# Kernel tuning notes

Hardware: AMD Instinct MI355X
Metric: run time of the kernel (lower is better)

Reference implementation:

```python
import jax, jax.numpy as jnp
import numpy as np

N = 50000      # nodes
E = 800000     # edges (avg degree 16)
F_IN = 128     # in_channels
H = 4          # heads
C = 32         # hidden_channels (per-head out)
L = 3          # num_layers
HC = H * C     # 128 == F_IN so residuals are active


def _layer_norm(x, g, b):
    mu = jnp.mean(x, axis=-1, keepdims=True)
    var = jnp.mean(jnp.square(x - mu), axis=-1, keepdims=True)
    return (x - mu) * jax.lax.rsqrt(var + 1e-5) * g + b


def _gatv2(x, W_l, b_l, W_r, b_r, att, src, dst, concat):
    # GATv2Conv (PyG semantics, eval mode: no dropout)
    xl = (x @ W_l + b_l).reshape(-1, H, C)   # source-side transform  [N,H,C]
    xr = (x @ W_r + b_r).reshape(-1, H, C)   # target-side transform  [N,H,C]
    e = jax.nn.leaky_relu(xl[src] + xr[dst], 0.2)          # [E,H,C]
    alpha = jnp.einsum('ehc,hc->eh', e, att)               # [E,H]
    # segment softmax over incoming edges of each dst node
    m = jax.ops.segment_max(alpha, dst, num_segments=N)    # [N,H]
    a = jnp.exp(alpha - m[dst])
    den = jax.ops.segment_sum(a, dst, num_segments=N) + 1e-16
    a = a / den[dst]
    out = jax.ops.segment_sum(xl[src] * a[:, :, None], dst, num_segments=N)  # [N,H,C]
    if concat:
        return out.reshape(N, HC)
    return out.mean(axis=1)


def setup_inputs() -> dict:
    key = jax.random.key(0)
    ks = jax.random.split(key, 6)
    s = 0.05
    return {
        "x": jax.random.normal(ks[0], (N, F_IN), jnp.float32),
        "edge_index": jax.random.randint(ks[1], (2, E), 0, N, dtype=jnp.int32),
        # all 3 layers have in=128, out=H*C=128 for the linears
        "Wl": jax.random.normal(ks[2], (L, F_IN, HC), jnp.float32) * s,
        "bl": jnp.zeros((L, HC), jnp.float32),
        "Wr": jax.random.normal(ks[3], (L, F_IN, HC), jnp.float32) * s,
        "br": jnp.zeros((L, HC), jnp.float32),
        "att": jax.random.normal(ks[4], (L, H, C), jnp.float32) * s,
        "out_bias01": jnp.zeros((2, HC), jnp.float32),   # concat layers 0,1
        "out_bias2": jnp.zeros((C,), jnp.float32),       # mean layer 2
        "ln_g01": jnp.ones((2, HC), jnp.float32),
        "ln_b01": jnp.zeros((2, HC), jnp.float32),
        "ln_g2": jnp.ones((C,), jnp.float32),
        "ln_b2": jnp.zeros((C,), jnp.float32),
    }


def reference(x, edge_index, Wl, bl, Wr, br, att,
              out_bias01, out_bias2, ln_g01, ln_b01, ln_g2, ln_b2):
    src, dst = edge_index[0], edge_index[1]
    for i in range(L):
        x_in = x
        concat = i < L - 1
        h = _gatv2(x, Wl[i], bl[i], Wr[i], br[i], att[i], src, dst, concat)
        if concat:
            h = h + out_bias01[i]
            h = _layer_norm(h, ln_g01[i], ln_b01[i])
        else:
            h = h + out_bias2
            h = _layer_norm(h, ln_g2, ln_b2)
        h = jax.nn.relu(h)  # dropout omitted (eval mode)
        if i > 0 and h.shape == x_in.shape:
            h = h + x_in
        x = h
    return x
```

## Files before the change

kernel.cpp:

```cpp
#include <hip/hip_runtime.h>
#include <math.h>


#define DPP_QP_XOR1 0xB1
#define DPP_QP_XOR2 0x4E
#define DPP_ROW_MIRROR 0x140
#define DPP_ROW_HALF_MIRROR 0x141

#define EPB 8192
#define MAXB 512
#define ECAP 4096
#define SCAP 4096

template <int CTRL>
__device__ __forceinline__ float dpp_add(float v) {
    int x = __builtin_amdgcn_update_dpp(0, __float_as_int(v), CTRL, 0xf, 0xf, true);
    return v + __int_as_float(x);
}

__device__ __forceinline__ unsigned bf16s(float f) {
    unsigned u = __float_as_uint(f);
    return (u + 0x7fffu + ((u >> 16) & 1u)) >> 16;
}

typedef __bf16 bf16x8 __attribute__((ext_vector_type(8)));
typedef float f32x4 __attribute__((ext_vector_type(4)));
typedef float f32x2 __attribute__((ext_vector_type(2)));


__global__ __launch_bounds__(256) void bin_kernel(
    const int* __restrict__ src, const int* __restrict__ dst,
    int* __restrict__ bucket_count, unsigned* __restrict__ ebuf,
    int E, int NB)
{
    __shared__ int hist[MAXB], lbase[MAXB], gbase[MAXB], cur[MAXB];
    __shared__ int sscan[256];
    __shared__ unsigned stage[EPB];
    const int t = threadIdx.x;
    const int base = blockIdx.x * EPB;
    const int cnt = min(EPB, E - base);

    for (int b = t; b < MAXB; b += 256) hist[b] = 0;
    __syncthreads();
    for (int idx = t; idx < cnt; idx += 256)
        atomicAdd(&hist[dst[base + idx] >> 7], 1);
    __syncthreads();
    {
        const int a = hist[2 * t], b = hist[2 * t + 1];
        sscan[t] = a + b;
        __syncthreads();
        for (int off = 1; off < 256; off <<= 1) {
            int u = (t >= off) ? sscan[t - off] : 0;
            __syncthreads();
            sscan[t] += u;
            __syncthreads();
        }
        const int ex = sscan[t] - (a + b);
        lbase[2 * t] = ex;
        lbase[2 * t + 1] = ex + a;
    }
    __syncthreads();
    for (int b = t; b < NB; b += 256) {
        const int c = hist[b];
        gbase[b] = (c > 0) ? atomicAdd(&bucket_count[b], c) : 0;
        cur[b] = lbase[b];
    }
    __syncthreads();
    for (int idx = t; idx < cnt; idx += 256) {
        const int d = dst[base + idx];
        const int bk = d >> 7;
        const int lp = atomicAdd(&cur[bk], 1);
        stage[lp] = (unsigned)src[base + idx] | ((unsigned)(d & 127) << 16)
                  | ((unsigned)bk << 23);
    }
    __syncthreads();
    for (int idx = t; idx < cnt; idx += 256) {
        const unsigned v = stage[idx];
        const int bk = v >> 23;
        ebuf[(size_t)bk * ECAP + gbase[bk] + (idx - lbase[bk])] = v;
    }
}


__global__ __launch_bounds__(256) void place_kernel(
    const unsigned* __restrict__ ebuf, const int* __restrict__ bucket_count,
    int* __restrict__ row_start, int* __restrict__ deg,
    unsigned short* __restrict__ src_sorted, int Nn, int NB)
{
    __shared__ int hist[128], lexcl[128], cur[128], s[128];
    __shared__ int ptotS;
    __shared__ unsigned short stage[SCAP];
    const int b = blockIdx.x;
    const int t = threadIdx.x;
    const int node0 = b * 128;
    const int cnt = min(bucket_count[b], ECAP);
    const unsigned* eb = ebuf + (size_t)b * ECAP;

    if (t < 128) hist[t] = 0;
    __syncthreads();
    for (int i = t; i < cnt; i += 256)
        atomicAdd(&hist[(eb[i] >> 16) & 127], 1);
    __syncthreads();
    int pv = 0;
    if (t < 128) { pv = (hist[t] + 3) & ~3; s[t] = pv; }
    __syncthreads();
    for (int off = 1; off < 128; off <<= 1) {
        int u = (t >= off && t < 128) ? s[t - off] : 0;
        __syncthreads();
        if (t < 128) s[t] += u;
        __syncthreads();
    }
    if (t < 128) {
        lexcl[t] = s[t] - pv;
        cur[t] = s[t] - pv;
        const int n = node0 + t;
        if (n < Nn) {
            row_start[n] = b * SCAP + lexcl[t];
            deg[n] = hist[t];
        }
    }
    if (t == 127) ptotS = s[127];
    __syncthreads();
    const int ptot = ptotS;
    for (int i = t; i < ptot; i += 256) stage[i] = 0;
    __syncthreads();
    for (int i = t; i < cnt; i += 256) {
        const unsigned v = eb[i];
        const int lp = atomicAdd(&cur[(v >> 16) & 127], 1);
        stage[lp] = (unsigned short)(v & 0xffffu);
    }
    __syncthreads();
    for (int i = t; i < ptot; i += 256)
        src_sorted[(size_t)b * SCAP + i] = stage[i];
}


__global__ __launch_bounds__(256) void prep_kernel(
    const float* __restrict__ Wl, const float* __restrict__ Wr,
    unsigned short* __restrict__ Bt, int* __restrict__ bucket_cnt, int btTotal)
{
    const int idx = blockIdx.x * blockDim.x + threadIdx.x;
    if (idx < MAXB) bucket_cnt[idx] = 0;
    if (idx < btTotal) {
        const int k = idx & 127;
        const int n = (idx >> 7) & 255;
        const int l = idx >> 15;
        const float v = (n < 128) ? Wl[l * 16384 + k * 128 + n]
                                  : Wr[l * 16384 + k * 128 + (n - 128)];
        Bt[idx] = (unsigned short)bf16s(v);
    }
}


template <bool F32A>
__global__ __launch_bounds__(256) void gemm_mfma(
    const void* __restrict__ Xv, const unsigned short* __restrict__ Bt,
    const float* __restrict__ bl, const float* __restrict__ br,
    unsigned short* __restrict__ XLb, unsigned short* __restrict__ XRb, int Nn)
{
    const int t = threadIdx.x;
    const int lane = t & 63;
    const int w = t >> 6;
    const int n0 = w * 64;
    const int l15 = lane & 15;
    const int kg = lane >> 4;
    const int rowBase = blockIdx.x * 32;

    f32x4 acc[2][4] = {};

    int ra[2];
    ra[0] = min(rowBase + l15, Nn - 1);
    ra[1] = min(rowBase + 16 + l15, Nn - 1);

#pragma unroll
    for (int ks = 0; ks < 4; ++ks) {
        const int k0 = ks * 32 + kg * 8;
        bf16x8 a[2];
#pragma unroll
        for (int mt = 0; mt < 2; ++mt) {
            if constexpr (F32A) {
                const float* X = (const float*)Xv;
                const float4 f0 = *reinterpret_cast<const float4*>(X + (size_t)ra[mt] * 128 + k0);
                const float4 f1 = *reinterpret_cast<const float4*>(X + (size_t)ra[mt] * 128 + k0 + 4);
                bf16x8 av;
                av[0] = (__bf16)f0.x; av[1] = (__bf16)f0.y;
                av[2] = (__bf16)f0.z; av[3] = (__bf16)f0.w;
                av[4] = (__bf16)f1.x; av[5] = (__bf16)f1.y;
                av[6] = (__bf16)f1.z; av[7] = (__bf16)f1.w;
                a[mt] = av;
            } else {
                const unsigned short* Xb = (const unsigned short*)Xv;
                a[mt] = *reinterpret_cast<const bf16x8*>(Xb + (size_t)ra[mt] * 128 + k0);
            }
        }
#pragma unroll
        for (int nt = 0; nt < 4; ++nt) {
            const int col = n0 + nt * 16 + l15;
            const bf16x8 b = *reinterpret_cast<const bf16x8*>(Bt + (size_t)col * 128 + k0);
            acc[0][nt] = __builtin_amdgcn_mfma_f32_16x16x32_bf16(a[0], b, acc[0][nt], 0, 0, 0);
            acc[1][nt] = __builtin_amdgcn_mfma_f32_16x16x32_bf16(a[1], b, acc[1][nt], 0, 0, 0);
        }
    }

    const bool isXL = (w < 2);
#pragma unroll
    for (int mt = 0; mt < 2; ++mt) {
#pragma unroll
        for (int nt = 0; nt < 4; ++nt) {
            const int col = n0 + nt * 16 + l15;
            const float bv = isXL ? bl[col] : br[col - 128];
#pragma unroll
            for (int r = 0; r < 4; ++r) {
                const int row = rowBase + mt * 16 + kg * 4 + r;
                if (row >= Nn) continue;
                const float v = acc[mt][nt][r] + bv;
                if (isXL) XLb[(size_t)row * 128 + col] = (unsigned short)bf16s(v);
                else      XRb[(size_t)row * 128 + (col - 128)] = (unsigned short)bf16s(v);
            }
        }
    }
}


__device__ __forceinline__ void unpack8(const uint4 q, f32x2* v) {
    v[0] = f32x2{__uint_as_float(q.x << 16), __uint_as_float(q.x & 0xffff0000u)};
    v[1] = f32x2{__uint_as_float(q.y << 16), __uint_as_float(q.y & 0xffff0000u)};
    v[2] = f32x2{__uint_as_float(q.z << 16), __uint_as_float(q.z & 0xffff0000u)};
    v[3] = f32x2{__uint_as_float(q.w << 16), __uint_as_float(q.w & 0xffff0000u)};
}

__device__ __forceinline__ void edge_accum(const uint4 q, const f32x2* xr, const f32x2* av,
                                           const bool dead, float& wsum, f32x2* acc) {
    f32x2 xl[4];
    unpack8(q, xl);
    f32x2 pd = {0.f, 0.f};
#pragma unroll
    for (int j = 0; j < 4; ++j) {
        f32x2 tt = xl[j] + xr[j];
        tt = __builtin_elementwise_max(tt, tt * 0.2f);
        pd += tt * av[j];
    }
    float part = pd.x + pd.y;
    part = dpp_add<DPP_QP_XOR1>(part);
    part = dpp_add<DPP_QP_XOR2>(part);
    if (dead) part = -INFINITY;
    const float e = __expf(part);
    wsum += e;
    const f32x2 e2 = {e, e};
#pragma unroll
    for (int j = 0; j < 4; ++j) acc[j] += e2 * xl[j];
}

template <int MODE>
__global__ __launch_bounds__(256, 8) void aggregate_kernel(
    const unsigned* __restrict__ XLb, const unsigned* __restrict__ XRb,
    const int* __restrict__ row_start, const int* __restrict__ deg,
    const unsigned short* __restrict__ src_sorted,
    const float* __restrict__ att, const float* __restrict__ obias,
    const float* __restrict__ lng, const float* __restrict__ lnb,
    const unsigned* __restrict__ residb, float* __restrict__ out,
    unsigned* __restrict__ outb, int Nn)
{
    const int lane = threadIdx.x & 63;
    const int wid = threadIdx.x >> 6;
    const int node = blockIdx.x * 4 + wid;
    if (node >= Nn) return;
    const int g = lane >> 4;
    const int i = lane & 15;
    const int c0 = i * 8;

    f32x2 xr[4], av[4];
    {
        const uint4 qr = reinterpret_cast<const uint4*>(XRb)[(size_t)node * 16 + i];
        unpack8(qr, xr);
        const float4 c = *reinterpret_cast<const float4*>(att + c0);
        const float4 d = *reinterpret_cast<const float4*>(att + c0 + 4);
        av[0] = f32x2{c.x, c.y}; av[1] = f32x2{c.z, c.w};
        av[2] = f32x2{d.x, d.y}; av[3] = f32x2{d.z, d.w};
    }

    f32x2 acc[4] = {};
    float wsum = 0.f;

    const int p0 = row_start[node];
    const int dg = deg[node];
    const int p1 = p0 + dg;
    const uint4* XL4 = reinterpret_cast<const uint4*>(XLb);

    if (dg > 0) {
        uint4 qA = XL4[(size_t)src_sorted[p0 + g] * 16 + i];
        uint4 qB = XL4[(size_t)src_sorted[p0 + 4 + g] * 16 + i];
        for (int p = p0; p < p1; p += 8) {
            const int sAn = src_sorted[p + 8 + g];
            const int sBn = src_sorted[p + 12 + g];
            const uint4 qAn = XL4[(size_t)sAn * 16 + i];
            const uint4 qBn = XL4[(size_t)sBn * 16 + i];
            edge_accum(qA, xr, av, p + g >= p1, wsum, acc);
            if (p + 4 < p1)
                edge_accum(qB, xr, av, p + 4 + g >= p1, wsum, acc);
            qA = qAn;
            qB = qBn;
        }
    }

    wsum += __shfl_xor(wsum, 16); wsum += __shfl_xor(wsum, 32);
    float o[8];
#pragma unroll
    for (int j = 0; j < 4; ++j) { o[2 * j] = acc[j].x; o[2 * j + 1] = acc[j].y; }
#pragma unroll
    for (int j = 0; j < 8; ++j) {
        o[j] += __shfl_xor(o[j], 16);
        o[j] += __shfl_xor(o[j], 32);
    }

    const float inv = 1.f / (wsum + 1e-16f);
#pragma unroll
    for (int j = 0; j < 8; ++j) o[j] *= inv;

    if (MODE < 2) {
        float v[8], d[8];
        float s = 0.f;
#pragma unroll
        for (int j = 0; j < 8; ++j) { v[j] = o[j] + obias[c0 + j]; s += v[j]; }
        s = dpp_add<DPP_QP_XOR1>(s); s = dpp_add<DPP_QP_XOR2>(s);
        s = dpp_add<DPP_ROW_MIRROR>(s); s = dpp_add<DPP_ROW_HALF_MIRROR>(s);
        const float mu = s * (1.f / 128.f);
        float q = 0.f;
#pragma unroll
        for (int j = 0; j < 8; ++j) { d[j] = v[j] - mu; q = fmaf(d[j], d[j], q); }
        q = dpp_add<DPP_QP_XOR1>(q); q = dpp_add<DPP_QP_XOR2>(q);
        q = dpp_add<DPP_ROW_MIRROR>(q); q = dpp_add<DPP_ROW_HALF_MIRROR>(q);
        const float rstd = rsqrtf(q * (1.f / 128.f) + 1e-5f);
        float h[8];
#pragma unroll
        for (int j = 0; j < 8; ++j)
            h[j] = fmaxf(d[j] * rstd * lng[c0 + j] + lnb[c0 + j], 0.f);
        if (MODE == 1) {
            const uint4 qr2 = reinterpret_cast<const uint4*>(residb)[(size_t)node * 16 + i];
            f32x2 rr[4];
            unpack8(qr2, rr);
            h[0] += rr[0].x; h[1] += rr[0].y; h[2] += rr[1].x; h[3] += rr[1].y;
            h[4] += rr[2].x; h[5] += rr[2].y; h[6] += rr[3].x; h[7] += rr[3].y;
        }
        if (g == 0) {
            uint4 pb;
            pb.x = bf16s(h[0]) | (bf16s(h[1]) << 16);
            pb.y = bf16s(h[2]) | (bf16s(h[3]) << 16);
            pb.z = bf16s(h[4]) | (bf16s(h[5]) << 16);
            pb.w = bf16s(h[6]) | (bf16s(h[7]) << 16);
            reinterpret_cast<uint4*>(outb)[(size_t)node * 16 + i] = pb;
        }
    } else {
#pragma unroll
        for (int j = 0; j < 8; ++j) {
            o[j] += __shfl_xor(o[j], 4);
            o[j] += __shfl_xor(o[j], 8);
            o[j] *= 0.25f;
        }
        const int cb = (i & 3) * 8;
        float v[8], d[8];
        float s = 0.f;
#pragma unroll
        for (int j = 0; j < 8; ++j) { v[j] = o[j] + obias[cb + j]; s += v[j]; }
        s = dpp_add<DPP_QP_XOR1>(s); s = dpp_add<DPP_QP_XOR2>(s);
        const float mu = s * (1.f / 32.f);
        float q = 0.f;
#pragma unroll
        for (int j = 0; j < 8; ++j) { d[j] = v[j] - mu; q = fmaf(d[j], d[j], q); }
        q = dpp_add<DPP_QP_XOR1>(q); q = dpp_add<DPP_QP_XOR2>(q);
        const float rstd = rsqrtf(q * (1.f / 32.f) + 1e-5f);
        float h[8];
#pragma unroll
        for (int j = 0; j < 8; ++j)
            h[j] = fmaxf(d[j] * rstd * lng[cb + j] + lnb[cb + j], 0.f);
        if (lane < 4) {
            *reinterpret_cast<float4*>(out + (size_t)node * 32 + cb) =
                make_float4(h[0], h[1], h[2], h[3]);
            *reinterpret_cast<float4*>(out + (size_t)node * 32 + cb + 4) =
                make_float4(h[4], h[5], h[6], h[7]);
        }
    }
}

extern "C" void kernel_launch(void* const* d_in, const int* in_sizes, int n_in,
                              void* d_out, int out_size, void* d_ws, size_t ws_size,
                              hipStream_t stream)
{
    const float* x    = (const float*)d_in[0];
    const int*   ei   = (const int*)d_in[1];
    const float* Wl   = (const float*)d_in[2];
    const float* bl   = (const float*)d_in[3];
    const float* Wr   = (const float*)d_in[4];
    const float* br   = (const float*)d_in[5];
    const float* att  = (const float*)d_in[6];
    const float* ob01 = (const float*)d_in[7];
    const float* ob2  = (const float*)d_in[8];
    const float* lg01 = (const float*)d_in[9];
    const float* lb01 = (const float*)d_in[10];
    const float* lg2  = (const float*)d_in[11];
    const float* lb2  = (const float*)d_in[12];
    float* outp = (float*)d_out;

    const int Nn = in_sizes[0] / 128;
    const int E  = in_sizes[1] / 2;
    const int* srcI = ei;
    const int* dstI = ei + E;
    const int NB = (Nn + 127) / 128;

    char* ws = (char*)d_ws;
    size_t off = 0;
    auto alloc = [&](size_t bytes) {
        void* p = ws + off;
        off += (bytes + 255) & ~(size_t)255;
        return p;
    };
    unsigned short* XLb   = (unsigned short*)alloc((size_t)Nn * 128 * 2);
    unsigned short* XRb   = (unsigned short*)alloc((size_t)Nn * 128 * 2);
    unsigned short* bufAb = (unsigned short*)alloc((size_t)Nn * 128 * 2);
    unsigned short* bufBb = (unsigned short*)alloc((size_t)Nn * 128 * 2);
    unsigned short* Bt    = (unsigned short*)alloc((size_t)3 * 256 * 128 * 2);
    int*   row_start      = (int*)alloc((size_t)Nn * 4);
    int*   deg            = (int*)alloc((size_t)Nn * 4);
    unsigned short* src_sorted = (unsigned short*)alloc((size_t)NB * SCAP * 2 + 256);
    unsigned* ebuf        = (unsigned*)alloc((size_t)NB * ECAP * 4);
    int*   bucket_cnt     = (int*)alloc((size_t)MAXB * 4);
    (void)ws_size;

    const int btTotal = 3 * 256 * 128;

    prep_kernel<<<(btTotal + 255) / 256, 256, 0, stream>>>(Wl, Wr, Bt, bucket_cnt, btTotal);
    bin_kernel<<<(E + EPB - 1) / EPB, 256, 0, stream>>>(srcI, dstI, bucket_cnt, ebuf, E, NB);
    place_kernel<<<NB, 256, 0, stream>>>(ebuf, bucket_cnt, row_start, deg, src_sorted, Nn, NB);

    const int gemm_grid = (Nn + 31) / 32;
    const int agg_grid  = (Nn + 3) / 4;

    gemm_mfma<true><<<gemm_grid, 256, 0, stream>>>(x, Bt, bl, br, XLb, XRb, Nn);
    aggregate_kernel<0><<<agg_grid, 256, 0, stream>>>((const unsigned*)XLb, (const unsigned*)XRb,
        row_start, deg, src_sorted, att, ob01, lg01, lb01, nullptr, nullptr,
        (unsigned*)bufAb, Nn);

    gemm_mfma<false><<<gemm_grid, 256, 0, stream>>>(bufAb, Bt + 32768, bl + 128, br + 128,
                                                    XLb, XRb, Nn);
    aggregate_kernel<1><<<agg_grid, 256, 0, stream>>>((const unsigned*)XLb, (const unsigned*)XRb,
        row_start, deg, src_sorted, att + 128, ob01 + 128, lg01 + 128, lb01 + 128,
        (const unsigned*)bufAb, nullptr, (unsigned*)bufBb, Nn);

    gemm_mfma<false><<<gemm_grid, 256, 0, stream>>>(bufBb, Bt + 65536, bl + 256, br + 256,
                                                    XLb, XRb, Nn);
    aggregate_kernel<2><<<agg_grid, 256, 0, stream>>>((const unsigned*)XLb, (const unsigned*)XRb,
        row_start, deg, src_sorted, att + 256, ob2, lg2, lb2, nullptr, outp, nullptr, Nn);
}
```

Measured before the change: 271.4 us.

## Vectorize GEMM epilogue stores and restructure aggregate prefetch to index-only

```diff
diff --git a/kernel.cpp b/kernel.cpp
--- a/kernel.cpp
+++ b/kernel.cpp
@@ -143,10 +143,15 @@
     if (idx < MAXB) bucket_cnt[idx] = 0;
     if (idx < btTotal) {
         const int k = idx & 127;
-        const int n = (idx >> 7) & 255;
+        const int slot = (idx >> 7) & 255;
         const int l = idx >> 15;
-        const float v = (n < 128) ? Wl[l * 16384 + k * 128 + n]
-                                  : Wr[l * 16384 + k * 128 + (n - 128)];
+        const int w = slot >> 6;
+        const int r6 = slot & 63;
+        const int nt = r6 >> 4;
+        const int l15 = r6 & 15;
+        const int nreal = w * 64 + l15 * 4 + nt;
+        const float v = (nreal < 128) ? Wl[l * 16384 + k * 128 + nreal]
+                                      : Wr[l * 16384 + k * 128 + (nreal - 128)];
         Bt[idx] = (unsigned short)bf16s(v);
     }
 }
@@ -195,28 +200,29 @@
         }
 #pragma unroll
         for (int nt = 0; nt < 4; ++nt) {
-            const int col = n0 + nt * 16 + l15;
-            const bf16x8 b = *reinterpret_cast<const bf16x8*>(Bt + (size_t)col * 128 + k0);
+            const int slot = n0 + nt * 16 + l15;
+            const bf16x8 b = *reinterpret_cast<const bf16x8*>(Bt + (size_t)slot * 128 + k0);
             acc[0][nt] = __builtin_amdgcn_mfma_f32_16x16x32_bf16(a[0], b, acc[0][nt], 0, 0, 0);
             acc[1][nt] = __builtin_amdgcn_mfma_f32_16x16x32_bf16(a[1], b, acc[1][nt], 0, 0, 0);
         }
     }
 
     const bool isXL = (w < 2);
+    const int cbase = (isXL ? n0 : n0 - 128) + l15 * 4;
+    const float* bias = isXL ? (bl + n0) : (br + (n0 - 128));
+    const float4 bv = *reinterpret_cast<const float4*>(bias + l15 * 4);
+    unsigned short* outp = isXL ? XLb : XRb;
+
 #pragma unroll
     for (int mt = 0; mt < 2; ++mt) {
 #pragma unroll
-        for (int nt = 0; nt < 4; ++nt) {
-            const int col = n0 + nt * 16 + l15;
-            const float bv = isXL ? bl[col] : br[col - 128];
-#pragma unroll
-            for (int r = 0; r < 4; ++r) {
-                const int row = rowBase + mt * 16 + kg * 4 + r;
-                if (row >= Nn) continue;
-                const float v = acc[mt][nt][r] + bv;
-                if (isXL) XLb[(size_t)row * 128 + col] = (unsigned short)bf16s(v);
-                else      XRb[(size_t)row * 128 + (col - 128)] = (unsigned short)bf16s(v);
-            }
+        for (int r = 0; r < 4; ++r) {
+            const int row = rowBase + mt * 16 + kg * 4 + r;
+            if (row >= Nn) continue;
+            uint2 u;
+            u.x = bf16s(acc[mt][0][r] + bv.x) | (bf16s(acc[mt][1][r] + bv.y) << 16);
+            u.y = bf16s(acc[mt][2][r] + bv.z) | (bf16s(acc[mt][3][r] + bv.w) << 16);
+            *reinterpret_cast<uint2*>(outp + (size_t)row * 128 + cbase) = u;
         }
     }
 }
@@ -252,7 +258,7 @@
 }
 
 template <int MODE>
-__global__ __launch_bounds__(256, 8) void aggregate_kernel(
+__global__ __launch_bounds__(256) void aggregate_kernel(
     const unsigned* __restrict__ XLb, const unsigned* __restrict__ XRb,
     const int* __restrict__ row_start, const int* __restrict__ deg,
     const unsigned short* __restrict__ src_sorted,
@@ -288,18 +294,19 @@
     const uint4* XL4 = reinterpret_cast<const uint4*>(XLb);
 
     if (dg > 0) {
-        uint4 qA = XL4[(size_t)src_sorted[p0 + g] * 16 + i];
-        uint4 qB = XL4[(size_t)src_sorted[p0 + 4 + g] * 16 + i];
+        int sA = src_sorted[min(p0 + g, p1 - 1)];
+        int sB = src_sorted[min(p0 + 4 + g, p1 - 1)];
         for (int p = p0; p < p1; p += 8) {
-            const int sAn = src_sorted[p + 8 + g];
-            const int sBn = src_sorted[p + 12 + g];
-            const uint4 qAn = XL4[(size_t)sAn * 16 + i];
-            const uint4 qBn = XL4[(size_t)sBn * 16 + i];
+            const int sAn = src_sorted[min(p + 8 + g, p1 - 1)];
+            const int sBn = src_sorted[min(p + 12 + g, p1 - 1)];
+            const uint4 qA = XL4[(size_t)sA * 16 + i];
             edge_accum(qA, xr, av, p + g >= p1, wsum, acc);
-            if (p + 4 < p1)
+            if (p + 4 < p1) {
+                const uint4 qB = XL4[(size_t)sB * 16 + i];
                 edge_accum(qB, xr, av, p + 4 + g >= p1, wsum, acc);
-            qA = qAn;
-            qB = qBn;
+            }
+            sA = sAn;
+            sB = sBn;
         }
     }
 
```

Measured after the change: 247.0 us. 9.0% less time.
